# Optimization experiments

Hardware: AMD Instinct MI355X
Metric: run time of the kernel (lower is better)

The kernel has to match this reference:

```python
import jax, jax.numpy as jnp
import numpy as np

B, N, D, H, DK, DV, E = 32, 512, 128, 8, 16, 16, 128
MLP_H = 16


def _uniform(key, shape, fan):
    s = 1.0 / np.sqrt(fan)
    return jax.random.uniform(key, shape, jnp.float32, -s, s)


def setup_inputs() -> dict:
    key = jax.random.key(0)
    ks = jax.random.split(key, 13)
    q = jax.random.normal(ks[0], (B, N, D), jnp.float32)
    mask = jax.random.randint(ks[1], (B, N, N), 0, 2) > 0  # True = attention not allowed
    edge_matrix = jax.random.normal(ks[2], (B, N, N), jnp.float32)
    # per-head projection weights (init: uniform(-1/sqrt(last_dim), ...))
    W_query = _uniform(ks[3], (H, D, DK), DK)
    W_key = _uniform(ks[4], (H, D, DK), DK)
    W_val = _uniform(ks[5], (H, D, DV), DV)
    W_out = _uniform(ks[6], (H, DV, E), E)
    # edge MLP: 1 -> 16 -> 16 -> n_heads, ReLU between layers
    mlp_W1 = _uniform(ks[7], (1, MLP_H), 1)
    mlp_b1 = _uniform(ks[8], (MLP_H,), 1)
    mlp_W2 = _uniform(ks[9], (MLP_H, MLP_H), MLP_H)
    mlp_b2 = _uniform(ks[10], (MLP_H,), MLP_H)
    mlp_W3 = _uniform(ks[11], (MLP_H, H), MLP_H)
    mlp_b3 = _uniform(ks[12], (H,), MLP_H)
    return dict(q=q, mask=mask, edge_matrix=edge_matrix,
                W_query=W_query, W_key=W_key, W_val=W_val, W_out=W_out,
                mlp_W1=mlp_W1, mlp_b1=mlp_b1, mlp_W2=mlp_W2, mlp_b2=mlp_b2,
                mlp_W3=mlp_W3, mlp_b3=mlp_b3)


def reference(q, mask, edge_matrix, W_query, W_key, W_val, W_out,
              mlp_W1, mlp_b1, mlp_W2, mlp_b2, mlp_W3, mlp_b3):
    dk = W_query.shape[-1]
    norm = 1.0 / np.sqrt(dk)
    # per-head projections: [H,B,N,dk]
    Q = jnp.einsum('bni,hid->hbnd', q, W_query)
    K = jnp.einsum('bni,hid->hbnd', q, W_key)
    V = jnp.einsum('bni,hid->hbnd', q, W_val)
    # scaled QK^T: [H,B,N,N]
    comp = norm * jnp.einsum('hbqd,hbkd->hbqk', Q, K)
    # edge-bias MLP on each scalar edge weight: [B,N,N,1] -> [B,N,N,H]
    e = edge_matrix[..., None]
    h1 = jax.nn.relu(e @ mlp_W1 + mlp_b1)
    h2 = jax.nn.relu(h1 @ mlp_W2 + mlp_b2)
    bias = h2 @ mlp_W3 + mlp_b3
    comp = comp + jnp.transpose(bias, (3, 0, 1, 2))
    # masked softmax (mask True = disallowed)
    m = mask[None]  # broadcast over heads
    comp = jnp.where(m, -jnp.inf, comp)
    attn = jax.nn.softmax(comp, axis=-1)
    attn = jnp.where(m, 0.0, attn)
    heads = jnp.einsum('hbqk,hbkd->hbqd', attn, V)  # [H,B,N,dv]
    out = jnp.einsum('hbqd,hde->bqe', heads, W_out)  # [B,N,E]
    return out
```

## Files before the change

### kernel.cpp

```cpp
#include <hip/hip_runtime.h>
#include <hip/hip_bf16.h>
#include <float.h>

#define Bc 32
#define Nc 512
#define Dc 128
#define Hc 8
#define DKc 16
#define Ec 128
#define LOG2E 1.44269504088896340736f

typedef __attribute__((ext_vector_type(4))) short s16x4;
typedef __attribute__((ext_vector_type(8))) short s16x8;
typedef __attribute__((ext_vector_type(4))) float f32x4;

union BFU { __hip_bfloat16 b; short s; };
static __device__ inline short f2bf(float f) { BFU u; u.b = __float2bfloat16(f); return u.s; }
static __device__ inline s16x4 pack4(float a, float b, float c, float d) {
  s16x4 r; r[0] = f2bf(a); r[1] = f2bf(b); r[2] = f2bf(c); r[3] = f2bf(d); return r;
}

#if __has_builtin(__builtin_amdgcn_exp2f)
#define EXP2F(x) __builtin_amdgcn_exp2f(x)
#else
#define EXP2F(x) exp2f(x)
#endif

static __device__ inline f32x4 mfma16(s16x4 a, s16x4 b, f32x4 c) {
#if __has_builtin(__builtin_amdgcn_mfma_f32_16x16x16bf16_1k)
  return __builtin_amdgcn_mfma_f32_16x16x16bf16_1k(a, b, c, 0, 0, 0);
#else
  int lane = threadIdx.x & 63;
  int g = lane >> 4, base = lane & 15;
  int src0 = (base + 32 * g) & 63;
  int src1 = (base + 32 * g + 16) & 63;
  int ax = ((int*)&a)[0], ay = ((int*)&a)[1];
  int bx = ((int*)&b)[0], by = ((int*)&b)[1];
  int A0 = __shfl(ax, src0), A1 = __shfl(ay, src0);
  int A2 = __shfl(ax, src1), A3 = __shfl(ay, src1);
  int B0 = __shfl(bx, src0), B1 = __shfl(by, src0);
  int B2 = __shfl(bx, src1), B3 = __shfl(by, src1);
  if (g >= 2) { A0 = A1 = A2 = A3 = 0; B0 = B1 = B2 = B3 = 0; }
  s16x8 A8, B8;
  ((int*)&A8)[0] = A0; ((int*)&A8)[1] = A1; ((int*)&A8)[2] = A2; ((int*)&A8)[3] = A3;
  ((int*)&B8)[0] = B0; ((int*)&B8)[1] = B1; ((int*)&B8)[2] = B2; ((int*)&B8)[3] = B3;
  return __builtin_amdgcn_mfma_f32_16x16x32_bf16(A8, B8, c, 0, 0, 0);
#endif
}

__global__ void detect_mask_kernel(const unsigned char* __restrict__ m, int* __restrict__ flag) {
  int t = threadIdx.x;
  int any = 0;
  for (int u = t; u < 16384; u += 256)
    if ((u & 3) != 0 && m[u] != 0) any = 1;
  unsigned long long bal = __ballot(any != 0);
  if ((t & 63) == 0 && bal != 0ULL) atomicOr(flag, 1);
}

__global__ __launch_bounds__(256) void convert_w(
    const float* __restrict__ Wq, const float* __restrict__ Wk, const float* __restrict__ Wv,
    short* __restrict__ Wt)
{
  int o = blockIdx.x * 256 + threadIdx.x;
  int mat = o >> 14, r = o & 16383;
  int hk = r >> 7, d = r & 127;
  const float* src = (mat == 0) ? Wq : ((mat == 1) ? Wk : Wv);
  Wt[o] = f2bf(src[(hk >> 4) * 2048 + d * 16 + (hk & 15)]);
}

__global__ __launch_bounds__(256) void qkv_proj3(
    const float* __restrict__ q, const short* __restrict__ Wt,
    short* __restrict__ Qb, short* __restrict__ Kb, short* __restrict__ Vt)
{
  __shared__ short qs[64][136];
  int blk = blockIdx.x;
  int b = blk >> 3;
  int rt = (blk & 7) * 64;
  int t = threadIdx.x;
  int wid = t >> 6, lane = t & 63;
  int lq = lane & 15, lg = lane >> 4;
  int rowb = wid * 16;

  for (int u = t; u < 2048; u += 256) {
    int row = u >> 5, c4 = (u & 31) * 4;
    float4 v = *(const float4*)&q[(((b << 9) + rt + row) << 7) + c4];
    s16x4 pk = pack4(v.x, v.y, v.z, v.w);
    *(s16x4*)&qs[row][c4] = pk;
  }
  __syncthreads();

  #pragma unroll 1
  for (int pj = 0; pj < 3; ++pj) {
    const short* Wm = Wt + pj * 16384;
    f32x4 acc[8];
    #pragma unroll
    for (int ct = 0; ct < 8; ++ct) acc[ct] = (f32x4)0.f;

    #pragma unroll 1
    for (int ks = 0; ks < 8; ++ks) {
      s16x4 af = *(const s16x4*)&qs[rowb + lq][ks * 16 + lg * 4];
      #pragma unroll
      for (int ct = 0; ct < 8; ++ct) {
        s16x4 bf = *(const s16x4*)&Wm[(ct * 16 + lq) * 128 + ks * 16 + lg * 4];
        acc[ct] = mfma16(af, bf, acc[ct]);
      }
    }

    if (pj == 0) {
      #pragma unroll
      for (int ct = 0; ct < 8; ++ct)
        #pragma unroll
        for (int r = 0; r < 4; ++r)
          Qb[(ct << 18) + (b << 13) + ((rt + rowb + lg * 4 + r) << 4) + lq] =
              f2bf(acc[ct][r] * (0.25f * LOG2E));
    } else if (pj == 1) {
      #pragma unroll
      for (int ct = 0; ct < 8; ++ct)
        #pragma unroll
        for (int r = 0; r < 4; ++r)
          Kb[(ct << 18) + (b << 13) + ((rt + rowb + lg * 4 + r) << 4) + lq] = f2bf(acc[ct][r]);
    } else {
      #pragma unroll
      for (int ct = 0; ct < 8; ++ct) {
        s16x4 pk = pack4(acc[ct][0], acc[ct][1], acc[ct][2], acc[ct][3]);
        *(s16x4*)&Vt[(ct << 18) + (((b << 4) + lq) << 9) + rt + rowb + lg * 4] = pk;
      }
    }
  }
}

__global__ __launch_bounds__(256, 4) void attn_fused3(
    const float* __restrict__ edge, const unsigned char* __restrict__ maskB,
    const int* __restrict__ flag,
    const short* __restrict__ Qb, const short* __restrict__ Kb, const short* __restrict__ Vt,
    const float* __restrict__ Wout,
    const float* __restrict__ mW1, const float* __restrict__ mb1,
    const float* __restrict__ mW2, const float* __restrict__ mb2,
    const float* __restrict__ mW3, const float* __restrict__ mb3,
    float* __restrict__ out)
{
  __shared__ float bias_s[4][2176];
  __shared__ float etile[4][16][16];

  int t = threadIdx.x;
  int wid = t >> 6, lane = t & 63;
  int lq = lane & 15, lg = lane >> 4;
  int b = blockIdx.x >> 5;
  int qt = (blockIdx.x & 31) * 16;
  int mflag = *flag;

  float W1v[4], b1v[4];
  f32x4 b2v, b3v;
  s16x4 w2f, w3f;
  #pragma unroll
  for (int i = 0; i < 4; ++i) {
    int v = lg * 4 + i;
    W1v[i] = mW1[v];
    b1v[i] = mb1[v];
    b2v[i] = mb2[v];
    b3v[i] = (v < 8) ? mb3[v] * LOG2E : 0.f;
    w2f[i] = f2bf(mW2[v * 16 + lq]);
    w3f[i] = (lq < 8) ? f2bf(mW3[v * 8 + lq] * LOG2E) : (short)0;
  }

  const short* Kl = Kb + (b << 13) + (lq << 4) + (lg << 2);
  const short* Vl = Vt + (((b << 4) + lq) << 9) + (lg << 2);
  const short* Ql = Qb + (b << 13) + ((qt + lq) << 4) + (lg << 2);
  unsigned ebase = (((b << 9) + qt + (lane >> 2)) << 9) + (lane & 3) * 4;
  unsigned mbase = (((b << 9) + qt + lq) << 9) + (lg << 2);

  s16x4 qf[8];
  #pragma unroll
  for (int h = 0; h < 8; ++h) qf[h] = *(const s16x4*)(Ql + (h << 18));

  f32x4 oacc[8];
  float psum[8];
  #pragma unroll
  for (int h = 0; h < 8; ++h) { oacc[h] = (f32x4)0.f; psum[h] = 0.f; }

  float* bw = &bias_s[wid][0];

  int jb = wid << 4;
  float4 ev = *(const float4*)&edge[ebase + jb];
  int4 mkv;
  if (mflag) {
    uchar4 u = *(const uchar4*)&maskB[mbase + jb];
    mkv.x = u.x; mkv.y = u.y; mkv.z = u.z; mkv.w = u.w;
  } else {
    mkv = *(const int4*)&((const int*)maskB)[mbase + jb];
  }

  #pragma unroll 1
  for (int cc = 0; cc < 8; ++cc) {
    jb = ((cc << 2) | wid) << 4;
    *(float4*)&etile[wid][lane >> 2][(lane & 3) * 4] = ev;

    float4 evn; int4 mkn;
    if (cc < 7) {
      int jbn = (((cc + 1) << 2) | wid) << 4;
      evn = *(const float4*)&edge[ebase + jbn];
      if (mflag) {
        uchar4 u = *(const uchar4*)&maskB[mbase + jbn];
        mkn.x = u.x; mkn.y = u.y; mkn.z = u.z; mkn.w = u.w;
      } else {
        mkn = *(const int4*)&((const int*)maskB)[mbase + jbn];
      }
    } else { evn = ev; mkn = mkv; }

    s16x4 kf[8];
    #pragma unroll
    for (int h = 0; h < 8; ++h) kf[h] = *(const s16x4*)(Kl + (h << 18) + (jb << 4));

    #pragma unroll 4
    for (int qq = 0; qq < 16; ++qq) {
      float e = etile[wid][qq][lq];
      s16x4 h1f = pack4(fmaxf(0.f, fmaf(e, W1v[0], b1v[0])),
                        fmaxf(0.f, fmaf(e, W1v[1], b1v[1])),
                        fmaxf(0.f, fmaf(e, W1v[2], b1v[2])),
                        fmaxf(0.f, fmaf(e, W1v[3], b1v[3])));
      f32x4 c2 = mfma16(w2f, h1f, b2v);
      s16x4 rf = pack4(fmaxf(c2[0], 0.f), fmaxf(c2[1], 0.f),
                       fmaxf(c2[2], 0.f), fmaxf(c2[3], 0.f));
      f32x4 c3 = mfma16(w3f, rf, b3v);
      if (lg < 2) {
        #pragma unroll
        for (int r = 0; r < 4; ++r)
          bw[lq * 130 + (lg * 4 + r) * 16 + qq] = c3[r];
      }
    }

    #pragma unroll
    for (int h = 0; h < 8; ++h) {
      f32x4 sc;
      #pragma unroll
      for (int r = 0; r < 4; ++r)
        sc[r] = bw[(lg * 4 + r) * 130 + h * 16 + lq];
      sc = mfma16(kf[h], qf[h], sc);
      s16x4 vf = *(const s16x4*)(Vl + (h << 18) + jb);
      float p0 = mkv.x ? 0.f : EXP2F(sc[0]);
      float p1 = mkv.y ? 0.f : EXP2F(sc[1]);
      float p2 = mkv.z ? 0.f : EXP2F(sc[2]);
      float p3 = mkv.w ? 0.f : EXP2F(sc[3]);
      psum[h] += (p0 + p1) + (p2 + p3);
      s16x4 pf = pack4(p0, p1, p2, p3);
      oacc[h] = mfma16(vf, pf, oacc[h]);
    }
    ev = evn; mkv = mkn;
  }

  __syncthreads();
  #pragma unroll
  for (int h = 0; h < 8; ++h) {
    #pragma unroll
    for (int r = 0; r < 4; ++r)
      bw[(h * 16 + lg * 4 + r) * 16 + lq] = oacc[h][r];
    float s = psum[h];
    s += __shfl_xor(s, 16);
    s += __shfl_xor(s, 32);
    if (lane < 16) bw[2048 + h * 16 + lq] = s;
  }
  __syncthreads();

  for (int u = t; u < 2048; u += 256) {
    float a = bias_s[0][u] + bias_s[1][u] + bias_s[2][u] + bias_s[3][u];
    int si = 2048 + ((u >> 8) << 4) + (u & 15);
    float sm = bias_s[0][si] + bias_s[1][si] + bias_s[2][si] + bias_s[3][si];
    bias_s[0][u] = (sm != 0.f) ? a / sm : 0.f;
  }
  __syncthreads();

  {
    int e = t & 127, qh = t >> 7;
    float acc[8];
    #pragma unroll
    for (int i = 0; i < 8; ++i) acc[i] = 0.f;
    #pragma unroll 4
    for (int hd = 0; hd < 128; ++hd) {
      float wv = Wout[hd * Ec + e];
      const float* on = &bias_s[0][hd * 16 + qh * 8];
      #pragma unroll
      for (int i = 0; i < 8; ++i) acc[i] = fmaf(on[i], wv, acc[i]);
    }
    #pragma unroll
    for (int i = 0; i < 8; ++i)
      out[(((b << 9) + qt + qh * 8 + i) << 7) + e] = acc[i];
  }
}

extern "C" void kernel_launch(void* const* d_in, const int* in_sizes, int n_in,
                              void* d_out, int out_size, void* d_ws, size_t ws_size,
                              hipStream_t stream)
{
  const float* q    = (const float*)d_in[0];
  const unsigned char* mask = (const unsigned char*)d_in[1];
  const float* edge = (const float*)d_in[2];
  const float* Wq   = (const float*)d_in[3];
  const float* Wk   = (const float*)d_in[4];
  const float* Wv   = (const float*)d_in[5];
  const float* Wo   = (const float*)d_in[6];
  const float* mW1  = (const float*)d_in[7];
  const float* mb1  = (const float*)d_in[8];
  const float* mW2  = (const float*)d_in[9];
  const float* mb2  = (const float*)d_in[10];
  const float* mW3  = (const float*)d_in[11];
  const float* mb3  = (const float*)d_in[12];
  float* out = (float*)d_out;

  size_t per = (size_t)Hc * Bc * Nc * DKc;
  short* Wt = (short*)d_ws;
  short* Qb = Wt + 49152;
  short* Kb = Qb + per;
  short* Vt = Kb + per;
  int* flag = (int*)(Vt + per);

  hipMemsetAsync(flag, 0, sizeof(int), stream);
  detect_mask_kernel<<<1, 256, 0, stream>>>(mask, flag);
  convert_w<<<dim3(192), dim3(256), 0, stream>>>(Wq, Wk, Wv, Wt);
  qkv_proj3<<<dim3(Bc * 8), dim3(256), 0, stream>>>(q, Wt, Qb, Kb, Vt);
  attn_fused3<<<dim3(Bc * 32), dim3(256), 0, stream>>>(edge, mask, flag, Qb, Kb, Vt, Wo,
      mW1, mb1, mW2, mb2, mW3, mb3, out);
}
```

Measured before the change: 132.3 us.

## Fuse prep kernels, use MFMA for output projection, store bias as bf16

Merges mask detection and weight conversion into one launch, which also produces a pre-swizzled bf16 W_out. The QKV projection now uses smaller 16-row tiles to launch more blocks. In the attention kernel the edge bias is stored in shared memory as bf16 with a new layout, shrinking LDS use. Softmax normalization is applied in registers, the final W_out projection runs on MFMA instead of scalar FMAs, and the exponent input is clamped. The changes lower launch count, LDS footprint and scalar epilogue cost, in exchange for bias precision loss and a cross-wave shared-memory reduction.

```diff
diff --git a/kernel.cpp b/kernel.cpp
--- a/kernel.cpp
+++ b/kernel.cpp
@@ -9,6 +9,7 @@
 #define DKc 16
 #define Ec 128
 #define LOG2E 1.44269504088896340736f
+#define SCLAMP 80.0f
 
 typedef __attribute__((ext_vector_type(4))) short s16x4;
 typedef __attribute__((ext_vector_type(8))) short s16x8;
@@ -48,106 +49,115 @@
 #endif
 }
 
-__global__ void detect_mask_kernel(const unsigned char* __restrict__ m, int* __restrict__ flag) {
+__global__ __launch_bounds__(256) void conv_detect(
+    const float* __restrict__ Wq, const float* __restrict__ Wk, const float* __restrict__ Wv,
+    const float* __restrict__ Wo,
+    const unsigned char* __restrict__ m, int* __restrict__ flag,
+    short* __restrict__ Wt, short* __restrict__ Wob)
+{
+  int blk = blockIdx.x;
   int t = threadIdx.x;
-  int any = 0;
-  for (int u = t; u < 16384; u += 256)
-    if ((u & 3) != 0 && m[u] != 0) any = 1;
-  unsigned long long bal = __ballot(any != 0);
-  if ((t & 63) == 0 && bal != 0ULL) atomicOr(flag, 1);
-}
-
-__global__ __launch_bounds__(256) void convert_w(
-    const float* __restrict__ Wq, const float* __restrict__ Wk, const float* __restrict__ Wv,
-    short* __restrict__ Wt)
-{
-  int o = blockIdx.x * 256 + threadIdx.x;
-  int mat = o >> 14, r = o & 16383;
-  int hk = r >> 7, d = r & 127;
-  const float* src = (mat == 0) ? Wq : ((mat == 1) ? Wk : Wv);
-  Wt[o] = f2bf(src[(hk >> 4) * 2048 + d * 16 + (hk & 15)]);
-}
-
-__global__ __launch_bounds__(256) void qkv_proj3(
+  if (blk == 256) {
+    int any = 0;
+    for (int u = t; u < 16384; u += 256)
+      if ((u & 3) != 0 && m[u] != 0) any = 1;
+    unsigned long long bal = __ballot(any != 0);
+    if ((t & 63) == 0 && bal != 0ULL) atomicOr(flag, 1);
+    return;
+  }
+  int o = blk * 256 + t;
+  if (o < 49152) {
+    int mat = o >> 14, r = o & 16383;
+    int hk = r >> 7, d = r & 127;
+    const float* src = (mat == 0) ? Wq : ((mat == 1) ? Wk : Wv);
+    Wt[o] = f2bf(src[(hk >> 4) * 2048 + d * 16 + (hk & 15)]);
+  } else {
+    int o2 = o - 49152;
+    int et = o2 >> 11, s = (o2 >> 8) & 7, lane = (o2 >> 2) & 63, i = o2 & 3;
+    Wob[o2] = f2bf(Wo[(s * 16 + (lane >> 4) * 4 + i) * 128 + et * 16 + (lane & 15)]);
+  }
+}
+
+__global__ __launch_bounds__(256, 4) void qkv4(
     const float* __restrict__ q, const short* __restrict__ Wt,
     short* __restrict__ Qb, short* __restrict__ Kb, short* __restrict__ Vt)
 {
-  __shared__ short qs[64][136];
+  __shared__ short qs[16][136];
   int blk = blockIdx.x;
-  int b = blk >> 3;
-  int rt = (blk & 7) * 64;
+  int b = blk >> 5;
+  int rt = (blk & 31) << 4;
   int t = threadIdx.x;
   int wid = t >> 6, lane = t & 63;
   int lq = lane & 15, lg = lane >> 4;
-  int rowb = wid * 16;
-
-  for (int u = t; u < 2048; u += 256) {
-    int row = u >> 5, c4 = (u & 31) * 4;
-    float4 v = *(const float4*)&q[(((b << 9) + rt + row) << 7) + c4];
-    s16x4 pk = pack4(v.x, v.y, v.z, v.w);
-    *(s16x4*)&qs[row][c4] = pk;
+
+  #pragma unroll
+  for (int it = 0; it < 2; ++it) {
+    int u = t + it * 256;
+    int row = u >> 5, c4 = (u & 31) << 2;
+    float4 v = *(const float4*)&q[((((b << 9) + rt + row) << 7)) + c4];
+    *(s16x4*)&qs[row][c4] = pack4(v.x, v.y, v.z, v.w);
   }
   __syncthreads();
+
+  s16x4 af[8];
+  #pragma unroll
+  for (int ks = 0; ks < 8; ++ks)
+    af[ks] = *(const s16x4*)&qs[lq][ks * 16 + lg * 4];
 
   #pragma unroll 1
   for (int pj = 0; pj < 3; ++pj) {
     const short* Wm = Wt + pj * 16384;
-    f32x4 acc[8];
-    #pragma unroll
-    for (int ct = 0; ct < 8; ++ct) acc[ct] = (f32x4)0.f;
-
-    #pragma unroll 1
-    for (int ks = 0; ks < 8; ++ks) {
-      s16x4 af = *(const s16x4*)&qs[rowb + lq][ks * 16 + lg * 4];
+    #pragma unroll
+    for (int c2 = 0; c2 < 2; ++c2) {
+      int ct = wid * 2 + c2;
+      f32x4 acc = (f32x4)0.f;
       #pragma unroll
-      for (int ct = 0; ct < 8; ++ct) {
+      for (int ks = 0; ks < 8; ++ks) {
         s16x4 bf = *(const s16x4*)&Wm[(ct * 16 + lq) * 128 + ks * 16 + lg * 4];
-        acc[ct] = mfma16(af, bf, acc[ct]);
+        acc = mfma16(af[ks], bf, acc);
       }
-    }
-
-    if (pj == 0) {
-      #pragma unroll
-      for (int ct = 0; ct < 8; ++ct)
+      if (pj == 0) {
+        s16x4 pk = pack4(acc[0] * (0.25f * LOG2E), acc[1] * (0.25f * LOG2E),
+                         acc[2] * (0.25f * LOG2E), acc[3] * (0.25f * LOG2E));
         #pragma unroll
         for (int r = 0; r < 4; ++r)
-          Qb[(ct << 18) + (b << 13) + ((rt + rowb + lg * 4 + r) << 4) + lq] =
-              f2bf(acc[ct][r] * (0.25f * LOG2E));
-    } else if (pj == 1) {
-      #pragma unroll
-      for (int ct = 0; ct < 8; ++ct)
+          Qb[(ct << 18) + (b << 13) + ((rt + lg * 4 + r) << 4) + lq] = pk[r];
+      } else if (pj == 1) {
+        s16x4 pk = pack4(acc[0], acc[1], acc[2], acc[3]);
         #pragma unroll
         for (int r = 0; r < 4; ++r)
-          Kb[(ct << 18) + (b << 13) + ((rt + rowb + lg * 4 + r) << 4) + lq] = f2bf(acc[ct][r]);
-    } else {
-      #pragma unroll
-      for (int ct = 0; ct < 8; ++ct) {
-        s16x4 pk = pack4(acc[ct][0], acc[ct][1], acc[ct][2], acc[ct][3]);
-        *(s16x4*)&Vt[(ct << 18) + (((b << 4) + lq) << 9) + rt + rowb + lg * 4] = pk;
+          Kb[(ct << 18) + (b << 13) + ((rt + lg * 4 + r) << 4) + lq] = pk[r];
+      } else {
+        s16x4 pk = pack4(acc[0], acc[1], acc[2], acc[3]);
+        *(s16x4*)&Vt[(ct << 18) + (((b << 4) + lq) << 9) + rt + lg * 4] = pk;
       }
     }
   }
 }
 
-__global__ __launch_bounds__(256, 4) void attn_fused3(
+__global__ __launch_bounds__(256, 4) void attn5(
     const float* __restrict__ edge, const unsigned char* __restrict__ maskB,
     const int* __restrict__ flag,
     const short* __restrict__ Qb, const short* __restrict__ Kb, const short* __restrict__ Vt,
-    const float* __restrict__ Wout,
+    const short* __restrict__ Wob,
     const float* __restrict__ mW1, const float* __restrict__ mb1,
     const float* __restrict__ mW2, const float* __restrict__ mb2,
     const float* __restrict__ mW3, const float* __restrict__ mb3,
     float* __restrict__ out)
 {
-  __shared__ float bias_s[4][2176];
-  __shared__ float etile[4][16][16];
+  __shared__ __align__(16) char smem[36864];
 
   int t = threadIdx.x;
   int wid = t >> 6, lane = t & 63;
   int lq = lane & 15, lg = lane >> 4;
   int b = blockIdx.x >> 5;
-  int qt = (blockIdx.x & 31) * 16;
+  int qt = (blockIdx.x & 31) << 4;
   int mflag = *flag;
+
+  short* bias_w = (short*)(smem + wid * 5120);
+  float (*etile)[16] = (float(*)[16])(smem + 20480 + wid * 1024);
+  float* d2L = (float*)smem;
+  float* psL = (float*)(smem + 34816);
 
   float W1v[4], b1v[4];
   f32x4 b2v, b3v;
@@ -178,8 +188,6 @@
   #pragma unroll
   for (int h = 0; h < 8; ++h) { oacc[h] = (f32x4)0.f; psum[h] = 0.f; }
 
-  float* bw = &bias_s[wid][0];
-
   int jb = wid << 4;
   float4 ev = *(const float4*)&edge[ebase + jb];
   int4 mkv;
@@ -193,7 +201,7 @@
   #pragma unroll 1
   for (int cc = 0; cc < 8; ++cc) {
     jb = ((cc << 2) | wid) << 4;
-    *(float4*)&etile[wid][lane >> 2][(lane & 3) * 4] = ev;
+    *(float4*)&etile[lane >> 2][(lane & 3) * 4] = ev;
 
     float4 evn; int4 mkn;
     if (cc < 7) {
@@ -213,7 +221,7 @@
 
     #pragma unroll 4
     for (int qq = 0; qq < 16; ++qq) {
-      float e = etile[wid][qq][lq];
+      float e = etile[qq][lq];
       s16x4 h1f = pack4(fmaxf(0.f, fmaf(e, W1v[0], b1v[0])),
                         fmaxf(0.f, fmaf(e, W1v[1], b1v[1])),
                         fmaxf(0.f, fmaf(e, W1v[2], b1v[2])),
@@ -223,24 +231,28 @@
                        fmaxf(c2[2], 0.f), fmaxf(c2[3], 0.f));
       f32x4 c3 = mfma16(w3f, rf, b3v);
       if (lg < 2) {
+        s16x4 pk = pack4(c3[0], c3[1], c3[2], c3[3]);
         #pragma unroll
         for (int r = 0; r < 4; ++r)
-          bw[lq * 130 + (lg * 4 + r) * 16 + qq] = c3[r];
+          bias_w[(lg * 4 + r) * 320 + qq * 20 + lq] = pk[r];
       }
     }
 
     #pragma unroll
     for (int h = 0; h < 8; ++h) {
+      union { s16x4 v; int i[2]; } bb;
+      bb.v = *(const s16x4*)&bias_w[h * 320 + lq * 20 + lg * 4];
       f32x4 sc;
-      #pragma unroll
-      for (int r = 0; r < 4; ++r)
-        sc[r] = bw[(lg * 4 + r) * 130 + h * 16 + lq];
+      sc[0] = __int_as_float(bb.i[0] << 16);
+      sc[1] = __int_as_float(bb.i[0] & 0xffff0000);
+      sc[2] = __int_as_float(bb.i[1] << 16);
+      sc[3] = __int_as_float(bb.i[1] & 0xffff0000);
       sc = mfma16(kf[h], qf[h], sc);
       s16x4 vf = *(const s16x4*)(Vl + (h << 18) + jb);
-      float p0 = mkv.x ? 0.f : EXP2F(sc[0]);
-      float p1 = mkv.y ? 0.f : EXP2F(sc[1]);
-      float p2 = mkv.z ? 0.f : EXP2F(sc[2]);
-      float p3 = mkv.w ? 0.f : EXP2F(sc[3]);
+      float p0 = mkv.x ? 0.f : EXP2F(fminf(sc[0], SCLAMP));
+      float p1 = mkv.y ? 0.f : EXP2F(fminf(sc[1], SCLAMP));
+      float p2 = mkv.z ? 0.f : EXP2F(fminf(sc[2], SCLAMP));
+      float p3 = mkv.w ? 0.f : EXP2F(fminf(sc[3], SCLAMP));
       psum[h] += (p0 + p1) + (p2 + p3);
       s16x4 pf = pack4(p0, p1, p2, p3);
       oacc[h] = mfma16(vf, pf, oacc[h]);
@@ -248,42 +260,56 @@
     ev = evn; mkv = mkn;
   }
 
-  __syncthreads();
   #pragma unroll
   for (int h = 0; h < 8; ++h) {
-    #pragma unroll
-    for (int r = 0; r < 4; ++r)
-      bw[(h * 16 + lg * 4 + r) * 16 + lq] = oacc[h][r];
     float s = psum[h];
     s += __shfl_xor(s, 16);
     s += __shfl_xor(s, 32);
-    if (lane < 16) bw[2048 + h * 16 + lq] = s;
+    psum[h] = s;
+  }
+  if (lg == 0) {
+    #pragma unroll
+    for (int h = 0; h < 8; ++h) psL[wid * 128 + h * 16 + lq] = psum[h];
   }
   __syncthreads();
 
-  for (int u = t; u < 2048; u += 256) {
-    float a = bias_s[0][u] + bias_s[1][u] + bias_s[2][u] + bias_s[3][u];
-    int si = 2048 + ((u >> 8) << 4) + (u & 15);
-    float sm = bias_s[0][si] + bias_s[1][si] + bias_s[2][si] + bias_s[3][si];
-    bias_s[0][u] = (sm != 0.f) ? a / sm : 0.f;
-  }
+  s16x4 obf[8];
+  #pragma unroll
+  for (int h = 0; h < 8; ++h) {
+    float tot = psL[h * 16 + lq] + psL[128 + h * 16 + lq]
+              + psL[256 + h * 16 + lq] + psL[384 + h * 16 + lq];
+    float inv = (tot > 0.f) ? 1.f / tot : 0.f;
+    obf[h] = pack4(oacc[h][0] * inv, oacc[h][1] * inv, oacc[h][2] * inv, oacc[h][3] * inv);
+  }
+
+  f32x4 d2a[8];
+  #pragma unroll
+  for (int et = 0; et < 8; ++et) d2a[et] = (f32x4)0.f;
+  #pragma unroll
+  for (int s = 0; s < 8; ++s) {
+    #pragma unroll
+    for (int et = 0; et < 8; ++et) {
+      s16x4 wo = *(const s16x4*)&Wob[((et * 8 + s) << 8) + (lane << 2)];
+      d2a[et] = mfma16(wo, obf[s], d2a[et]);
+    }
+  }
+
+  #pragma unroll
+  for (int et = 0; et < 8; ++et)
+    #pragma unroll
+    for (int r = 0; r < 4; ++r)
+      d2L[(wid * 128 + et * 16 + lg * 4 + r) * 17 + lq] = d2a[et][r];
   __syncthreads();
 
-  {
-    int e = t & 127, qh = t >> 7;
-    float acc[8];
-    #pragma unroll
-    for (int i = 0; i < 8; ++i) acc[i] = 0.f;
-    #pragma unroll 4
-    for (int hd = 0; hd < 128; ++hd) {
-      float wv = Wout[hd * Ec + e];
-      const float* on = &bias_s[0][hd * 16 + qh * 8];
-      #pragma unroll
-      for (int i = 0; i < 8; ++i) acc[i] = fmaf(on[i], wv, acc[i]);
-    }
-    #pragma unroll
-    for (int i = 0; i < 8; ++i)
-      out[(((b << 9) + qt + qh * 8 + i) << 7) + e] = acc[i];
+  #pragma unroll
+  for (int k = 0; k < 2; ++k) {
+    int et = wid * 2 + k;
+    #pragma unroll
+    for (int r = 0; r < 4; ++r) {
+      int el = (et * 16 + lg * 4 + r) * 17 + lq;
+      float v = d2L[el] + d2L[2176 + el] + d2L[4352 + el] + d2L[6528 + el];
+      out[(((b << 9) + qt + lq) << 7) + et * 16 + lg * 4 + r] = v;
+    }
   }
 }
 
@@ -307,16 +333,16 @@
   float* out = (float*)d_out;
 
   size_t per = (size_t)Hc * Bc * Nc * DKc;
-  short* Wt = (short*)d_ws;
-  short* Qb = Wt + 49152;
-  short* Kb = Qb + per;
-  short* Vt = Kb + per;
-  int* flag = (int*)(Vt + per);
+  short* Wt  = (short*)d_ws;
+  short* Wob = Wt + 49152;
+  short* Qb  = Wob + 16384;
+  short* Kb  = Qb + per;
+  short* Vt  = Kb + per;
+  int* flag  = (int*)(Vt + per);
 
   hipMemsetAsync(flag, 0, sizeof(int), stream);
-  detect_mask_kernel<<<1, 256, 0, stream>>>(mask, flag);
-  convert_w<<<dim3(192), dim3(256), 0, stream>>>(Wq, Wk, Wv, Wt);
-  qkv_proj3<<<dim3(Bc * 8), dim3(256), 0, stream>>>(q, Wt, Qb, Kb, Vt);
-  attn_fused3<<<dim3(Bc * 32), dim3(256), 0, stream>>>(edge, mask, flag, Qb, Kb, Vt, Wo,
+  conv_detect<<<dim3(257), dim3(256), 0, stream>>>(Wq, Wk, Wv, Wo, mask, flag, Wt, Wob);
+  qkv4<<<dim3(Bc * 32), dim3(256), 0, stream>>>(q, Wt, Qb, Kb, Vt);
+  attn5<<<dim3(Bc * 32), dim3(256), 0, stream>>>(edge, mask, flag, Qb, Kb, Vt, Wob,
       mW1, mb1, mW2, mb2, mW3, mb3, out);
 }
```

Result: no change. 130.0 us (-1.7%).
